# Performance work log

Measured on AMD Instinct MI355X. Metric: run time of the kernel, lower is better.

The kernel has to match this reference:

```python
import jax, jax.numpy as jnp
import numpy as np

N_MODELS = 128
N_FEAT = 32
TREE_LAYERS = [64, 32, 16]
INPUT_SIZE = 512
BATCH = 8192
EPS = 1e-5


def _uniform(key, shape, fan_in, fan_out):
    stdv = np.sqrt(6.0 / (fan_in + fan_out))
    return jax.random.uniform(key, shape, jnp.float32, -stdv, stdv)


def setup_inputs() -> dict:
    key = jax.random.key(0)
    ks = jax.random.split(key, 8)
    x = jax.random.normal(ks[0], (BATCH, INPUT_SIZE), jnp.float32)
    # flattened per-tree feature indices, shape [n_models * n_feature]
    used_features = jax.random.randint(ks[1], (N_MODELS * N_FEAT,), 0, INPUT_SIZE, jnp.int32)
    W1 = _uniform(ks[2], (N_MODELS, N_FEAT, TREE_LAYERS[0]), N_FEAT, TREE_LAYERS[0])
    b1 = jnp.zeros((N_MODELS, 1, TREE_LAYERS[0]), jnp.float32)
    W2 = _uniform(ks[3], (N_MODELS, TREE_LAYERS[0], TREE_LAYERS[1]), TREE_LAYERS[0], TREE_LAYERS[1])
    b2 = jnp.zeros((N_MODELS, 1, TREE_LAYERS[1]), jnp.float32)
    W3 = _uniform(ks[4], (N_MODELS, TREE_LAYERS[1], TREE_LAYERS[2]), TREE_LAYERS[1], TREE_LAYERS[2])
    b3 = jnp.zeros((N_MODELS, 1, TREE_LAYERS[2]), jnp.float32)
    gamma1 = jnp.ones((N_MODELS * TREE_LAYERS[0],), jnp.float32)
    beta1 = jnp.zeros((N_MODELS * TREE_LAYERS[0],), jnp.float32)
    gamma2 = jnp.ones((N_MODELS * TREE_LAYERS[1],), jnp.float32)
    beta2 = jnp.zeros((N_MODELS * TREE_LAYERS[1],), jnp.float32)
    out_weight = jax.random.normal(ks[5], (N_MODELS * TREE_LAYERS[2], 1), jnp.float32)
    out_bias = jnp.zeros((1,), jnp.float32)
    return {
        "x": x, "used_features": used_features,
        "W1": W1, "b1": b1, "W2": W2, "b2": b2, "W3": W3, "b3": b3,
        "gamma1": gamma1, "beta1": beta1, "gamma2": gamma2, "beta2": beta2,
        "out_weight": out_weight, "out_bias": out_bias,
    }


def _batch_dense(h, W, b):
    # h: [B, n_models, in], W: [n_models, in, out], b: [n_models, 1, out]
    return jnp.einsum("bmi,mio->bmo", h, W) + b[None, :, 0, :]


def _batchnorm_train(z, gamma, beta):
    # BatchNorm1d in training mode over 2D input: per-feature batch stats (biased var)
    mean = jnp.mean(z, axis=0)
    var = jnp.var(z, axis=0)
    return (z - mean) * jax.lax.rsqrt(var + EPS) * gamma + beta


def reference(x, used_features, W1, b1, W2, b2, W3, b3,
              gamma1, beta1, gamma2, beta2, out_weight, out_bias):
    B = x.shape[0]
    # gather used features: [B, n_models * n_feature] -> [B, n_models, n_feature]
    h = x[:, used_features].reshape(B, N_MODELS, N_FEAT)
    # layer 1: grouped GEMM + BN + ReLU
    h = _batch_dense(h, W1, b1).reshape(B, -1)
    h = jax.nn.relu(_batchnorm_train(h, gamma1, beta1))
    # layer 2
    h = _batch_dense(h.reshape(B, N_MODELS, -1), W2, b2).reshape(B, -1)
    h = jax.nn.relu(_batchnorm_train(h, gamma2, beta2))
    # last layer (no BN/ReLU) -> pred
    pred = _batch_dense(h.reshape(B, N_MODELS, -1), W3, b3).reshape(B, -1)
    out = pred @ out_weight + out_bias
    return (out, pred)
```

## Files before the change

kernel.cpp:

```cpp
#include <hip/hip_runtime.h>
#include <hip/hip_bf16.h>

#define BATCH   8192
#define NM      128
#define NF      32
#define L1      64
#define L2O     32
#define L3O     16
#define INSZ    512
#define SB      16
#define RPC     (BATCH/SB)
#define EPSV    1e-5f
#define CH      16
#define PARTS   (CH*4)

typedef __attribute__((ext_vector_type(8))) short short8;
typedef __attribute__((ext_vector_type(4))) float f32x4;

__device__ inline unsigned short f2bf(float f) {
    union { float f; unsigned u; } v; v.f = f;
    unsigned r = (v.u + 0x7FFF + ((v.u >> 16) & 1)) >> 16;
    return (unsigned short)r;
}


__global__ __launch_bounds__(256) void k_gather(
    const float* __restrict__ x, const int* __restrict__ uf,
    unsigned short* __restrict__ Ag)
{
    __shared__ float xs[16*INSZ];
    __shared__ int   sUf[NM*NF];
    const int rb = blockIdx.x;
    const int t  = threadIdx.x;
    const float4* xsrc = (const float4*)(x + (size_t)rb*16*INSZ);
    float4* xdst = (float4*)xs;
    #pragma unroll
    for (int p = 0; p < 8; ++p) xdst[t + p*256] = xsrc[t + p*256];
    const int4* us = (const int4*)uf;
    int4* ud = (int4*)sUf;
    #pragma unroll
    for (int p = 0; p < 4; ++p) ud[t + p*256] = us[t + p*256];
    __syncthreads();
    unsigned* outp = (unsigned*)(Ag + (size_t)rb*NM*512);
    const int e = t*2, r = e >> 5, j = e & 31;
    for (int m = 0; m < NM; ++m) {
        const int i0 = sUf[m*NF + j], i1 = sUf[m*NF + j + 1];
        const float g0 = xs[r*INSZ + i0], g1 = xs[r*INSZ + i1];
        outp[m*256 + t] = (unsigned)f2bf(g0) | ((unsigned)f2bf(g1) << 16);
    }
}

__global__ __launch_bounds__(256) void k_stats1_m(
    const unsigned short* __restrict__ Ag, const float* __restrict__ W1,
    float* __restrict__ sum1p, float* __restrict__ sq1p)
{
    const int m = blockIdx.x >> 4, chunk = blockIdx.x & 15;
    const int t = threadIdx.x, w = t >> 6, l = t & 63;
    const int lr = l & 15, lg = l >> 4;
    short8 w1f[4];
    #pragma unroll
    for (int n = 0; n < 4; ++n)
        #pragma unroll
        for (int s = 0; s < 8; ++s)
            w1f[n][s] = (short)f2bf(W1[(size_t)m*NF*L1 + (lg*8+s)*L1 + n*16 + lr]);
    float sum[4] = {0,0,0,0}, sq[4] = {0,0,0,0};
    for (int i = 0; i < 8; ++i) {
        const int rbG = chunk*32 + i*4 + w;
        const short8 a = *(const short8*)(Ag + ((size_t)rbG*NM + m)*512 + lr*32 + lg*8);
        #pragma unroll
        for (int n = 0; n < 4; ++n) {
            f32x4 acc = {0.f,0.f,0.f,0.f};
            acc = __builtin_amdgcn_mfma_f32_16x16x32_bf16(a, w1f[n], acc, 0, 0, 0);
            sum[n] += (acc[0]+acc[1]) + (acc[2]+acc[3]);
            sq[n]  += acc[0]*acc[0] + acc[1]*acc[1] + acc[2]*acc[2] + acc[3]*acc[3];
        }
    }
    #pragma unroll
    for (int n = 0; n < 4; ++n) {
        sum[n] += __shfl_xor(sum[n], 16); sum[n] += __shfl_xor(sum[n], 32);
        sq[n]  += __shfl_xor(sq[n], 16);  sq[n]  += __shfl_xor(sq[n], 32);
    }
    if (l < 16) {
        const int slot = chunk*4 + w;
        #pragma unroll
        for (int n = 0; n < 4; ++n) {
            const int f = m*L1 + n*16 + l;
            sum1p[(size_t)f*PARTS + slot] = sum[n];
            sq1p [(size_t)f*PARTS + slot] = sq[n];
        }
    }
}

__global__ __launch_bounds__(256) void k_finalize_m(
    const float* __restrict__ sump, const float* __restrict__ sqp,
    const float* __restrict__ bias, const float* __restrict__ gamma,
    const float* __restrict__ beta, float* __restrict__ scale,
    float* __restrict__ shift, int nfeat)
{
    int f = blockIdx.x*256 + threadIdx.x;
    if (f >= nfeat) return;
    float S = 0.f, Q = 0.f;
    #pragma unroll 8
    for (int c = 0; c < PARTS; ++c) { S += sump[(size_t)f*PARTS+c]; Q += sqp[(size_t)f*PARTS+c]; }
    float mz   = S * (1.f/BATCH);
    float var  = Q * (1.f/BATCH) - mz*mz;
    float mean = mz + bias[f];
    float sc   = rsqrtf(var + EPSV) * gamma[f];
    scale[f] = sc; shift[f] = beta[f] - mean*sc;
}

__global__ __launch_bounds__(256) void k_stats2_m(
    const unsigned short* __restrict__ Ag, const float* __restrict__ W1,
    const float* __restrict__ scale1, const float* __restrict__ shift1,
    const float* __restrict__ W2,
    float* __restrict__ sum2p, float* __restrict__ sq2p)
{
    __shared__ unsigned short h1T[4][16*72];
    const int m = blockIdx.x >> 4, chunk = blockIdx.x & 15;
    const int t = threadIdx.x, w = t >> 6, l = t & 63;
    const int lr = l & 15, lg = l >> 4;
    short8 w1f[4];
    #pragma unroll
    for (int n = 0; n < 4; ++n)
        #pragma unroll
        for (int s = 0; s < 8; ++s)
            w1f[n][s] = (short)f2bf(W1[(size_t)m*NF*L1 + (lg*8+s)*L1 + n*16 + lr]);
    float sc1[4], sh1[4];
    #pragma unroll
    for (int n = 0; n < 4; ++n) {
        sc1[n] = scale1[m*L1 + n*16 + lr];
        sh1[n] = shift1[m*L1 + n*16 + lr];
    }
    short8 w2f[2][2];
    #pragma unroll
    for (int n2 = 0; n2 < 2; ++n2)
        #pragma unroll
        for (int ks = 0; ks < 2; ++ks)
            #pragma unroll
            for (int s = 0; s < 8; ++s)
                w2f[n2][ks][s] = (short)f2bf(W2[(size_t)m*L1*L2O + (ks*32+lg*8+s)*L2O + n2*16 + lr]);
    unsigned short* hT = &h1T[w][0];
    float sum[2] = {0,0}, sq[2] = {0,0};
    for (int i = 0; i < 8; ++i) {
        const int rbG = chunk*32 + i*4 + w;
        const short8 a = *(const short8*)(Ag + ((size_t)rbG*NM + m)*512 + lr*32 + lg*8);
        #pragma unroll
        for (int n = 0; n < 4; ++n) {
            f32x4 acc = {0.f,0.f,0.f,0.f};
            acc = __builtin_amdgcn_mfma_f32_16x16x32_bf16(a, w1f[n], acc, 0, 0, 0);
            #pragma unroll
            for (int r = 0; r < 4; ++r) {
                float h = acc[r]*sc1[n] + sh1[n];
                hT[(lg*4+r)*72 + n*16 + lr] = f2bf(h > 0.f ? h : 0.f);
            }
        }
        #pragma unroll
        for (int n2 = 0; n2 < 2; ++n2) {
            f32x4 acc = {0.f,0.f,0.f,0.f};
            #pragma unroll
            for (int ks = 0; ks < 2; ++ks) {
                const short8 a2 = *(const short8*)(hT + lr*72 + ks*32 + lg*8);
                acc = __builtin_amdgcn_mfma_f32_16x16x32_bf16(a2, w2f[n2][ks], acc, 0, 0, 0);
            }
            sum[n2] += (acc[0]+acc[1]) + (acc[2]+acc[3]);
            sq[n2]  += acc[0]*acc[0] + acc[1]*acc[1] + acc[2]*acc[2] + acc[3]*acc[3];
        }
    }
    #pragma unroll
    for (int n2 = 0; n2 < 2; ++n2) {
        sum[n2] += __shfl_xor(sum[n2], 16); sum[n2] += __shfl_xor(sum[n2], 32);
        sq[n2]  += __shfl_xor(sq[n2], 16);  sq[n2]  += __shfl_xor(sq[n2], 32);
    }
    if (l < 16) {
        const int slot = chunk*4 + w;
        #pragma unroll
        for (int n2 = 0; n2 < 2; ++n2) {
            const int f = m*L2O + n2*16 + l;
            sum2p[(size_t)f*PARTS + slot] = sum[n2];
            sq2p [(size_t)f*PARTS + slot] = sq[n2];
        }
    }
}

__global__ __launch_bounds__(256) void k_final_m(
    const unsigned short* __restrict__ Ag, const float* __restrict__ W1,
    const float* __restrict__ scale1, const float* __restrict__ shift1,
    const float* __restrict__ W2,
    const float* __restrict__ scale2, const float* __restrict__ shift2,
    const float* __restrict__ W3, const float* __restrict__ b3,
    const float* __restrict__ ow,
    float* __restrict__ pred, float* __restrict__ outpart)
{
    __shared__ unsigned short h1T[4][16*72];
    __shared__ unsigned short h2T[4][16*40];
    const int m = blockIdx.x >> 4, chunk = blockIdx.x & 15;
    const int t = threadIdx.x, w = t >> 6, l = t & 63;
    const int lr = l & 15, lg = l >> 4;
    short8 w1f[4];
    #pragma unroll
    for (int n = 0; n < 4; ++n)
        #pragma unroll
        for (int s = 0; s < 8; ++s)
            w1f[n][s] = (short)f2bf(W1[(size_t)m*NF*L1 + (lg*8+s)*L1 + n*16 + lr]);
    float sc1[4], sh1[4];
    #pragma unroll
    for (int n = 0; n < 4; ++n) {
        sc1[n] = scale1[m*L1 + n*16 + lr];
        sh1[n] = shift1[m*L1 + n*16 + lr];
    }
    short8 w2f[2][2];
    #pragma unroll
    for (int n2 = 0; n2 < 2; ++n2)
        #pragma unroll
        for (int ks = 0; ks < 2; ++ks)
            #pragma unroll
            for (int s = 0; s < 8; ++s)
                w2f[n2][ks][s] = (short)f2bf(W2[(size_t)m*L1*L2O + (ks*32+lg*8+s)*L2O + n2*16 + lr]);
    float sc2[2], sh2[2];
    #pragma unroll
    for (int n2 = 0; n2 < 2; ++n2) {
        sc2[n2] = scale2[m*L2O + n2*16 + lr];
        sh2[n2] = shift2[m*L2O + n2*16 + lr];
    }
    short8 w3f;
    #pragma unroll
    for (int s = 0; s < 8; ++s)
        w3f[s] = (short)f2bf(W3[(size_t)m*L2O*L3O + (lg*8+s)*L3O + lr]);
    const float b3v = b3[m*L3O + lr];
    const float owv = ow[m*L3O + lr];
    unsigned short* hT  = &h1T[w][0];
    unsigned short* hT2 = &h2T[w][0];
    for (int i = 0; i < 8; ++i) {
        const int rbG = chunk*32 + i*4 + w;
        const short8 a = *(const short8*)(Ag + ((size_t)rbG*NM + m)*512 + lr*32 + lg*8);
        #pragma unroll
        for (int n = 0; n < 4; ++n) {
            f32x4 acc = {0.f,0.f,0.f,0.f};
            acc = __builtin_amdgcn_mfma_f32_16x16x32_bf16(a, w1f[n], acc, 0, 0, 0);
            #pragma unroll
            for (int r = 0; r < 4; ++r) {
                float h = acc[r]*sc1[n] + sh1[n];
                hT[(lg*4+r)*72 + n*16 + lr] = f2bf(h > 0.f ? h : 0.f);
            }
        }
        #pragma unroll
        for (int n2 = 0; n2 < 2; ++n2) {
            f32x4 acc = {0.f,0.f,0.f,0.f};
            #pragma unroll
            for (int ks = 0; ks < 2; ++ks) {
                const short8 a2 = *(const short8*)(hT + lr*72 + ks*32 + lg*8);
                acc = __builtin_amdgcn_mfma_f32_16x16x32_bf16(a2, w2f[n2][ks], acc, 0, 0, 0);
            }
            #pragma unroll
            for (int r = 0; r < 4; ++r) {
                float h = acc[r]*sc2[n2] + sh2[n2];
                hT2[(lg*4+r)*40 + n2*16 + lr] = f2bf(h > 0.f ? h : 0.f);
            }
        }
        {
            const short8 a3 = *(const short8*)(hT2 + lr*40 + lg*8);
            f32x4 acc = {0.f,0.f,0.f,0.f};
            acc = __builtin_amdgcn_mfma_f32_16x16x32_bf16(a3, w3f, acc, 0, 0, 0);
            #pragma unroll
            for (int r = 0; r < 4; ++r) {
                const float pv = acc[r] + b3v;
                const size_t row = (size_t)rbG*16 + lg*4 + r;
                pred[row*(NM*L3O) + m*L3O + lr] = pv;
                float v = pv * owv;
                v += __shfl_xor(v, 1); v += __shfl_xor(v, 2);
                v += __shfl_xor(v, 4); v += __shfl_xor(v, 8);
                if (lr == 0) outpart[row*NM + m] = v;
            }
        }
    }
}


__global__ __launch_bounds__(256) void k_stats1(
    const float* __restrict__ x, const int* __restrict__ uf,
    const float* __restrict__ W1, const float* __restrict__ b1,
    float* __restrict__ sum1p, float* __restrict__ sq1p)
{
    __shared__ __align__(16) float sW1[NF*L1];
    __shared__ __align__(16) float sFeat[8][NF];
    __shared__ int sIdx[NF];
    __shared__ float sRed[L1][4][2];
    const int m = blockIdx.x >> 4;
    const int c = blockIdx.x & (SB-1);
    const int t = threadIdx.x;
    for (int i = t; i < NF*L1; i += 256) sW1[i] = W1[m*NF*L1 + i];
    if (t < NF) sIdx[t] = uf[m*NF + t];
    __syncthreads();
    const int o = t & 63, r = t >> 6;
    float wcol[NF];
    #pragma unroll
    for (int i = 0; i < NF; ++i) wcol[i] = sW1[i*L1 + o];
    const float bias = b1[m*L1 + o];
    float sum = 0.f, sq = 0.f;
    const int row0 = c * RPC;
    const int rr = t >> 5, j = t & 31;
    for (int stage = 0; stage < RPC/8; ++stage) {
        __syncthreads();
        sFeat[rr][j] = x[(row0 + stage*8 + rr)*INSZ + sIdx[j]];
        __syncthreads();
        #pragma unroll
        for (int k = 0; k < 2; ++k) {
            const float4* fv = (const float4*)(&sFeat[r + k*4][0]);
            float acc = bias;
            #pragma unroll
            for (int ii = 0; ii < NF/4; ++ii) {
                float4 f4 = fv[ii];
                acc += f4.x*wcol[ii*4+0] + f4.y*wcol[ii*4+1]
                     + f4.z*wcol[ii*4+2] + f4.w*wcol[ii*4+3];
            }
            sum += acc; sq += acc*acc;
        }
    }
    sRed[o][r][0] = sum; sRed[o][r][1] = sq;
    __syncthreads();
    if (t < L1) {
        float S = 0.f, Q = 0.f;
        #pragma unroll
        for (int g = 0; g < 4; ++g) { S += sRed[t][g][0]; Q += sRed[t][g][1]; }
        sum1p[(m*L1 + t)*SB + c] = S;
        sq1p [(m*L1 + t)*SB + c] = Q;
    }
}

__global__ __launch_bounds__(256) void k_finalize(
    const float* __restrict__ sump, const float* __restrict__ sqp,
    const float* __restrict__ gamma, const float* __restrict__ beta,
    float* __restrict__ scale, float* __restrict__ shift, int nfeat)
{
    int f = blockIdx.x*256 + threadIdx.x;
    if (f >= nfeat) return;
    float S = 0.f, Q = 0.f;
    #pragma unroll
    for (int c = 0; c < SB; ++c) { S += sump[f*SB + c]; Q += sqp[f*SB + c]; }
    float mean = S * (1.f/BATCH);
    float var  = Q * (1.f/BATCH) - mean*mean;
    float rstd = rsqrtf(var + EPSV);
    float sc = rstd * gamma[f];
    scale[f] = sc;
    shift[f] = beta[f] - mean*sc;
}

__global__ __launch_bounds__(256) void k_stats2(
    const float* __restrict__ x, const int* __restrict__ uf,
    const float* __restrict__ W1, const float* __restrict__ b1,
    const float* __restrict__ scale1, const float* __restrict__ shift1,
    const float* __restrict__ W2, const float* __restrict__ b2,
    float* __restrict__ sum2p, float* __restrict__ sq2p)
{
    __shared__ __align__(16) float sW1[NF*L1];
    __shared__ __align__(16) float sFeat[8][NF];
    __shared__ __align__(16) float sH1[8][L1];
    __shared__ int sIdx[NF];
    __shared__ float sB1[L1], sSc[L1], sSh[L1];
    __shared__ float sRed[L2O][8][2];
    const int m = blockIdx.x >> 4, c = blockIdx.x & 15, t = threadIdx.x;
    for (int i = t; i < NF*L1; i += 256) sW1[i] = W1[m*NF*L1 + i];
    if (t < NF) sIdx[t] = uf[m*NF + t];
    if (t < L1) { sB1[t] = b1[m*L1+t]; sSc[t] = scale1[m*L1+t]; sSh[t] = shift1[m*L1+t]; }
    const int o2 = t & 31, r8 = t >> 5;
    float wcol2[L1];
    #pragma unroll
    for (int i = 0; i < L1; ++i) wcol2[i] = W2[m*L1*L2O + i*L2O + o2];
    const float b2v = b2[m*L2O + o2];
    __syncthreads();
    const int o1 = t & 63, r4 = t >> 6;
    float wcol1[NF];
    #pragma unroll
    for (int i = 0; i < NF; ++i) wcol1[i] = sW1[i*L1 + o1];
    const float b1v = sB1[o1], scv = sSc[o1], shv = sSh[o1];
    float sum = 0.f, sq = 0.f;
    const int row0 = c * RPC;
    const int rr = t >> 5, j = t & 31;
    for (int stage = 0; stage < RPC/8; ++stage) {
        __syncthreads();
        sFeat[rr][j] = x[(row0 + stage*8 + rr)*INSZ + sIdx[j]];
        __syncthreads();
        #pragma unroll
        for (int k = 0; k < 2; ++k) {
            const int rrow = r4 + k*4;
            const float4* fv = (const float4*)(&sFeat[rrow][0]);
            float acc = b1v;
            #pragma unroll
            for (int ii = 0; ii < NF/4; ++ii) {
                float4 f4 = fv[ii];
                acc += f4.x*wcol1[ii*4+0] + f4.y*wcol1[ii*4+1]
                     + f4.z*wcol1[ii*4+2] + f4.w*wcol1[ii*4+3];
            }
            float h = acc*scv + shv;
            sH1[rrow][o1] = h > 0.f ? h : 0.f;
        }
        __syncthreads();
        {
            const float4* hv = (const float4*)(&sH1[r8][0]);
            float acc = b2v;
            #pragma unroll
            for (int ii = 0; ii < L1/4; ++ii) {
                float4 h4 = hv[ii];
                acc += h4.x*wcol2[ii*4+0] + h4.y*wcol2[ii*4+1]
                     + h4.z*wcol2[ii*4+2] + h4.w*wcol2[ii*4+3];
            }
            sum += acc; sq += acc*acc;
        }
    }
    sRed[o2][r8][0] = sum; sRed[o2][r8][1] = sq;
    __syncthreads();
    if (t < L2O) {
        float S = 0.f, Q = 0.f;
        #pragma unroll
        for (int g = 0; g < 8; ++g) { S += sRed[t][g][0]; Q += sRed[t][g][1]; }
        sum2p[(m*L2O + t)*SB + c] = S;
        sq2p [(m*L2O + t)*SB + c] = Q;
    }
}

__global__ __launch_bounds__(256) void k_final(
    const float* __restrict__ x, const int* __restrict__ uf,
    const float* __restrict__ W1, const float* __restrict__ b1,
    const float* __restrict__ scale1, const float* __restrict__ shift1,
    const float* __restrict__ W2, const float* __restrict__ b2,
    const float* __restrict__ scale2, const float* __restrict__ shift2,
    const float* __restrict__ W3, const float* __restrict__ b3,
    const float* __restrict__ ow,
    float* __restrict__ pred, float* __restrict__ outpart)
{
    __shared__ __align__(16) float sW1[NF*L1];
    __shared__ __align__(16) float sFeat[8][NF];
    __shared__ __align__(16) float sH1[8][L1];
    __shared__ __align__(16) float sH2[8][L2O];
    __shared__ float sOut[8][L3O];
    __shared__ int sIdx[NF];
    __shared__ float sB1[L1], sSc[L1], sSh[L1];
    const int m = blockIdx.x >> 4, c = blockIdx.x & 15, t = threadIdx.x;
    for (int i = t; i < NF*L1; i += 256) sW1[i] = W1[m*NF*L1 + i];
    if (t < NF) sIdx[t] = uf[m*NF + t];
    if (t < L1) { sB1[t] = b1[m*L1+t]; sSc[t] = scale1[m*L1+t]; sSh[t] = shift1[m*L1+t]; }
    const int o2 = t & 31, r8 = t >> 5;
    float wcol2[L1];
    #pragma unroll
    for (int i = 0; i < L1; ++i) wcol2[i] = W2[m*L1*L2O + i*L2O + o2];
    const float b2v = b2[m*L2O + o2];
    const float sc2 = scale2[m*L2O + o2], sh2 = shift2[m*L2O + o2];
    const int o3 = t & 15, r16 = t >> 4;
    float wcol3[NF];
    #pragma unroll
    for (int i = 0; i < L2O; ++i) wcol3[i] = W3[m*L2O*L3O + i*L3O + o3];
    const float b3v = b3[m*L3O + o3];
    const float owv = ow[m*L3O + o3];
    __syncthreads();
    const int o1 = t & 63, r4 = t >> 6;
    float wcol1[NF];
    #pragma unroll
    for (int i = 0; i < NF; ++i) wcol1[i] = sW1[i*L1 + o1];
    const float b1v = sB1[o1], scv = sSc[o1], shv = sSh[o1];
    const int row0 = c * RPC;
    const int rr = t >> 5, j = t & 31;
    for (int stage = 0; stage < RPC/8; ++stage) {
        __syncthreads();
        sFeat[rr][j] = x[(row0 + stage*8 + rr)*INSZ + sIdx[j]];
        __syncthreads();
        #pragma unroll
        for (int k = 0; k < 2; ++k) {
            const int rrow = r4 + k*4;
            const float4* fv = (const float4*)(&sFeat[rrow][0]);
            float acc = b1v;
            #pragma unroll
            for (int ii = 0; ii < NF/4; ++ii) {
                float4 f4 = fv[ii];
                acc += f4.x*wcol1[ii*4+0] + f4.y*wcol1[ii*4+1]
                     + f4.z*wcol1[ii*4+2] + f4.w*wcol1[ii*4+3];
            }
            float h = acc*scv + shv;
            sH1[rrow][o1] = h > 0.f ? h : 0.f;
        }
        __syncthreads();
        {
            const float4* hv = (const float4*)(&sH1[r8][0]);
            float acc = b2v;
            #pragma unroll
            for (int ii = 0; ii < L1/4; ++ii) {
                float4 h4 = hv[ii];
                acc += h4.x*wcol2[ii*4+0] + h4.y*wcol2[ii*4+1]
                     + h4.z*wcol2[ii*4+2] + h4.w*wcol2[ii*4+3];
            }
            float h = acc*sc2 + sh2;
            sH2[r8][o2] = h > 0.f ? h : 0.f;
        }
        __syncthreads();
        if (t < 128) {
            const float4* hv = (const float4*)(&sH2[r16][0]);
            float acc = b3v;
            #pragma unroll
            for (int ii = 0; ii < L2O/4; ++ii) {
                float4 h4 = hv[ii];
                acc += h4.x*wcol3[ii*4+0] + h4.y*wcol3[ii*4+1]
                     + h4.z*wcol3[ii*4+2] + h4.w*wcol3[ii*4+3];
            }
            const int row = row0 + stage*8 + r16;
            pred[row*(NM*L3O) + m*L3O + o3] = acc;
            sOut[r16][o3] = acc * owv;
        }
        __syncthreads();
        if (t < 8) {
            float s = 0.f;
            #pragma unroll
            for (int i = 0; i < L3O; ++i) s += sOut[t][i];
            outpart[(row0 + stage*8 + t)*NM + m] = s;
        }
    }
}

__global__ __launch_bounds__(256) void k_out(
    const float* __restrict__ outpart, const float* __restrict__ ob,
    float* __restrict__ out)
{
    int b = blockIdx.x*256 + threadIdx.x;
    if (b >= BATCH) return;
    const float4* p = (const float4*)(outpart + (size_t)b*NM);
    float acc = 0.f;
    #pragma unroll
    for (int i = 0; i < NM/4; ++i) { float4 v = p[i]; acc += v.x + v.y + v.z + v.w; }
    out[b] = acc + ob[0];
}

extern "C" void kernel_launch(void* const* d_in, const int* in_sizes, int n_in,
                              void* d_out, int out_size, void* d_ws, size_t ws_size,
                              hipStream_t stream) {
    const float* x   = (const float*)d_in[0];
    const int*   uf  = (const int*  )d_in[1];
    const float* W1  = (const float*)d_in[2];
    const float* b1  = (const float*)d_in[3];
    const float* W2  = (const float*)d_in[4];
    const float* b2  = (const float*)d_in[5];
    const float* W3  = (const float*)d_in[6];
    const float* b3  = (const float*)d_in[7];
    const float* g1  = (const float*)d_in[8];
    const float* be1 = (const float*)d_in[9];
    const float* g2  = (const float*)d_in[10];
    const float* be2 = (const float*)d_in[11];
    const float* ow  = (const float*)d_in[12];
    const float* ob  = (const float*)d_in[13];

    float* out  = (float*)d_out;
    float* pred = out + BATCH;

    const size_t agElems = (size_t)BATCH * NM * NF;
    size_t need = agElems * 2;
    need += (size_t)(NM*L1*PARTS) * 4 * 2;
    need += (size_t)(NM*L2O*PARTS) * 4 * 2;
    need += (size_t)(NM*L1) * 4 * 2 + (size_t)(NM*L2O) * 4 * 2;
    need += (size_t)BATCH * NM * 4;

    if (ws_size >= need) {
        unsigned short* Ag = (unsigned short*)d_ws;
        float* w = (float*)(Ag + agElems);
        float* sum1p  = w;  w += NM*L1*PARTS;
        float* sq1p   = w;  w += NM*L1*PARTS;
        float* sum2p  = w;  w += NM*L2O*PARTS;
        float* sq2p   = w;  w += NM*L2O*PARTS;
        float* scale1 = w;  w += NM*L1;
        float* shift1 = w;  w += NM*L1;
        float* scale2 = w;  w += NM*L2O;
        float* shift2 = w;  w += NM*L2O;
        float* outpart= w;  w += (size_t)BATCH*NM;

        k_gather<<<BATCH/16, 256, 0, stream>>>(x, uf, Ag);
        k_stats1_m<<<NM*CH, 256, 0, stream>>>(Ag, W1, sum1p, sq1p);
        k_finalize_m<<<(NM*L1+255)/256, 256, 0, stream>>>(sum1p, sq1p, b1, g1, be1, scale1, shift1, NM*L1);
        k_stats2_m<<<NM*CH, 256, 0, stream>>>(Ag, W1, scale1, shift1, W2, sum2p, sq2p);
        k_finalize_m<<<(NM*L2O+255)/256, 256, 0, stream>>>(sum2p, sq2p, b2, g2, be2, scale2, shift2, NM*L2O);
        k_final_m<<<NM*CH, 256, 0, stream>>>(Ag, W1, scale1, shift1, W2, scale2, shift2,
                                             W3, b3, ow, pred, outpart);
        k_out<<<BATCH/256, 256, 0, stream>>>(outpart, ob, out);
    } else {
        float* w = (float*)d_ws;
        float* sum1p  = w;  w += NM*L1*SB;
        float* sq1p   = w;  w += NM*L1*SB;
        float* scale1 = w;  w += NM*L1;
        float* shift1 = w;  w += NM*L1;
        float* sum2p  = w;  w += NM*L2O*SB;
        float* sq2p   = w;  w += NM*L2O*SB;
        float* scale2 = w;  w += NM*L2O;
        float* shift2 = w;  w += NM*L2O;
        float* outpart= w;  w += (size_t)BATCH*NM;

        k_stats1<<<NM*SB, 256, 0, stream>>>(x, uf, W1, b1, sum1p, sq1p);
        k_finalize<<<(NM*L1+255)/256, 256, 0, stream>>>(sum1p, sq1p, g1, be1, scale1, shift1, NM*L1);
        k_stats2<<<NM*SB, 256, 0, stream>>>(x, uf, W1, b1, scale1, shift1, W2, b2, sum2p, sq2p);
        k_finalize<<<(NM*L2O+255)/256, 256, 0, stream>>>(sum2p, sq2p, g2, be2, scale2, shift2, NM*L2O);
        k_final<<<NM*SB, 256, 0, stream>>>(x, uf, W1, b1, scale1, shift1, W2, b2,
                                           scale2, shift2, W3, b3, ow, pred, outpart);
        k_out<<<BATCH/256, 256, 0, stream>>>(outpart, ob, out);
    }
}
```

Baseline: 116.3 us.

## Fuse gather with layer-1 stats and prepack bf16 MFMA weight fragments

Adds a prep kernel that converts W1/W2/W3 to bf16 in MFMA fragment order once per call, so the stats and final kernels load a short8 directly instead of doing per-element float loads and conversions. The gather kernel now also computes the layer-1 BatchNorm partial sums, converting x to bf16 in shared memory, which removes the separate stats1 pass over Ag. The output partial buffer is stored model-major so the final reduction reads coalesced, and the old ws-less fallback path is removed. The cost is more partial slots (256) for the stats1 finalize and one extra small launch.

```diff
diff --git a/kernel.cpp b/kernel.cpp
--- a/kernel.cpp
+++ b/kernel.cpp
@@ -8,21 +8,299 @@
 #define L2O     32
 #define L3O     16
 #define INSZ    512
-#define SB      16
-#define RPC     (BATCH/SB)
 #define EPSV    1e-5f
 #define CH      16
-#define PARTS   (CH*4)
+#define P64     64
+#define GS1B    256
+#define XS_STR  522
 
 typedef __attribute__((ext_vector_type(8))) short short8;
 typedef __attribute__((ext_vector_type(4))) float f32x4;
 
+union U8 { short8 s8; unsigned u[4]; };
+
 __device__ inline unsigned short f2bf(float f) {
     union { float f; unsigned u; } v; v.f = f;
-    unsigned r = (v.u + 0x7FFF + ((v.u >> 16) & 1)) >> 16;
-    return (unsigned short)r;
-}
-
+    return (unsigned short)((v.u + 0x7FFF + ((v.u >> 16) & 1)) >> 16);
+}
+__device__ inline unsigned pkbf(float a, float b) {
+    union { __hip_bfloat162 h; unsigned u; } c;
+    c.h = __float22bfloat162_rn(float2{a, b});
+    return c.u;
+}
+
+__global__ __launch_bounds__(256) void k_prep(
+    const float* __restrict__ W1, const float* __restrict__ W2,
+    const float* __restrict__ W3,
+    unsigned short* __restrict__ W1p, unsigned short* __restrict__ W2p,
+    unsigned short* __restrict__ W3p)
+{
+    int g = blockIdx.x*256 + threadIdx.x;
+    int m = g / 4608, r = g % 4608;
+    if (r < 2048) {
+        int n = r >> 9, l = (r >> 3) & 63, s = r & 7;
+        W1p[m*2048 + r] = f2bf(W1[m*2048 + ((l>>4)*8+s)*L1 + n*16 + (l&15)]);
+    } else if (r < 4096) {
+        int q = r - 2048;
+        int f = q >> 9, l = (q >> 3) & 63, s = q & 7;
+        int n2 = f >> 1, ks = f & 1;
+        W2p[m*2048 + q] = f2bf(W2[m*2048 + (ks*32+(l>>4)*8+s)*L2O + n2*16 + (l&15)]);
+    } else {
+        int q = r - 4096;
+        int l = (q >> 3) & 63, s = q & 7;
+        W3p[m*512 + q] = f2bf(W3[m*512 + ((l>>4)*8+s)*L3O + (l&15)]);
+    }
+}
+
+__global__ __launch_bounds__(512) void k_gs1(
+    const float* __restrict__ x, const int* __restrict__ uf,
+    const unsigned short* __restrict__ W1p,
+    unsigned short* __restrict__ Ag,
+    float* __restrict__ s1sum, float* __restrict__ s1sq)
+{
+    __shared__ unsigned short xs[32*XS_STR];
+    __shared__ int sUf[NM*NF];
+    const int blk = blockIdx.x, t = threadIdx.x;
+    #pragma unroll
+    for (int p = 0; p < 8; ++p) {
+        const float4 v = *(const float4*)(x + (size_t)blk*32*INSZ + p*2048 + t*4);
+        const int row = 4*p + (t>>7), col = (t&127)*4;
+        *(unsigned*)(&xs[row*XS_STR + col])     = pkbf(v.x, v.y);
+        *(unsigned*)(&xs[row*XS_STR + col + 2]) = pkbf(v.z, v.w);
+    }
+    #pragma unroll
+    for (int p = 0; p < 2; ++p)
+        ((int4*)sUf)[t + p*512] = ((const int4*)uf)[t + p*512];
+    __syncthreads();
+
+    const int w = t >> 6, l = t & 63, lr = l & 15, lg = l >> 4;
+    const unsigned short* xr0 = xs + lr*XS_STR;
+    const unsigned short* xr1 = xs + (16+lr)*XS_STR;
+    for (int mi = 0; mi < 16; ++mi) {
+        const int m = w*16 + mi;
+        const int4 ia = ((const int4*)sUf)[m*8 + lg*2];
+        const int4 ib = ((const int4*)sUf)[m*8 + lg*2 + 1];
+        U8 A0, A1;
+        A0.u[0] = xr0[ia.x] | ((unsigned)xr0[ia.y] << 16);
+        A0.u[1] = xr0[ia.z] | ((unsigned)xr0[ia.w] << 16);
+        A0.u[2] = xr0[ib.x] | ((unsigned)xr0[ib.y] << 16);
+        A0.u[3] = xr0[ib.z] | ((unsigned)xr0[ib.w] << 16);
+        A1.u[0] = xr1[ia.x] | ((unsigned)xr1[ia.y] << 16);
+        A1.u[1] = xr1[ia.z] | ((unsigned)xr1[ia.w] << 16);
+        A1.u[2] = xr1[ib.x] | ((unsigned)xr1[ib.y] << 16);
+        A1.u[3] = xr1[ib.z] | ((unsigned)xr1[ib.w] << 16);
+        *(short8*)(Ag + ((size_t)(blk*2  )*NM + m)*512 + lr*32 + lg*8) = A0.s8;
+        *(short8*)(Ag + ((size_t)(blk*2+1)*NM + m)*512 + lr*32 + lg*8) = A1.s8;
+        float sum[4], sq[4];
+        #pragma unroll
+        for (int n = 0; n < 4; ++n) {
+            const short8 wf = *(const short8*)(W1p + m*2048 + n*512 + l*8);
+            f32x4 z = {0.f,0.f,0.f,0.f};
+            f32x4 c0 = __builtin_amdgcn_mfma_f32_16x16x32_bf16(A0.s8, wf, z, 0, 0, 0);
+            f32x4 c1 = __builtin_amdgcn_mfma_f32_16x16x32_bf16(A1.s8, wf, z, 0, 0, 0);
+            sum[n] = (c0[0]+c0[1]) + (c0[2]+c0[3]) + (c1[0]+c1[1]) + (c1[2]+c1[3]);
+            sq[n]  = c0[0]*c0[0] + c0[1]*c0[1] + c0[2]*c0[2] + c0[3]*c0[3]
+                   + c1[0]*c1[0] + c1[1]*c1[1] + c1[2]*c1[2] + c1[3]*c1[3];
+        }
+        #pragma unroll
+        for (int n = 0; n < 4; ++n) {
+            sum[n] += __shfl_xor(sum[n], 16); sum[n] += __shfl_xor(sum[n], 32);
+            sq[n]  += __shfl_xor(sq[n], 16);  sq[n]  += __shfl_xor(sq[n], 32);
+        }
+        if (l < 16) {
+            #pragma unroll
+            for (int n = 0; n < 4; ++n) {
+                s1sum[(size_t)blk*8192 + m*64 + n*16 + l] = sum[n];
+                s1sq [(size_t)blk*8192 + m*64 + n*16 + l] = sq[n];
+            }
+        }
+    }
+}
+
+__global__ __launch_bounds__(256) void k_fin(
+    const float* __restrict__ sump, const float* __restrict__ sqp,
+    const float* __restrict__ bias, const float* __restrict__ gamma,
+    const float* __restrict__ beta, float* __restrict__ scale,
+    float* __restrict__ shift, int nfeat, int parts, int slotMajor)
+{
+    int f = blockIdx.x*256 + threadIdx.x;
+    if (f >= nfeat) return;
+    float S = 0.f, Q = 0.f;
+    if (slotMajor) {
+        #pragma unroll 8
+        for (int c = 0; c < parts; ++c) { S += sump[(size_t)c*nfeat + f]; Q += sqp[(size_t)c*nfeat + f]; }
+    } else {
+        #pragma unroll 8
+        for (int c = 0; c < parts; ++c) { S += sump[(size_t)f*parts + c]; Q += sqp[(size_t)f*parts + c]; }
+    }
+    float mz   = S * (1.f/BATCH);
+    float var  = Q * (1.f/BATCH) - mz*mz;
+    float mean = mz + bias[f];
+    float sc   = rsqrtf(var + EPSV) * gamma[f];
+    scale[f] = sc; shift[f] = beta[f] - mean*sc;
+}
+
+__global__ __launch_bounds__(256) void k_stats2_p(
+    const unsigned short* __restrict__ Ag, const unsigned short* __restrict__ W1p,
+    const float* __restrict__ scale1, const float* __restrict__ shift1,
+    const unsigned short* __restrict__ W2p,
+    float* __restrict__ sum2p, float* __restrict__ sq2p)
+{
+    __shared__ unsigned short h1T[4][16*72];
+    const int m = blockIdx.x >> 4, chunk = blockIdx.x & 15;
+    const int t = threadIdx.x, w = t >> 6, l = t & 63;
+    const int lr = l & 15, lg = l >> 4;
+    short8 w1f[4];
+    #pragma unroll
+    for (int n = 0; n < 4; ++n) w1f[n] = *(const short8*)(W1p + m*2048 + n*512 + l*8);
+    short8 w2f[2][2];
+    #pragma unroll
+    for (int n2 = 0; n2 < 2; ++n2)
+        #pragma unroll
+        for (int ks = 0; ks < 2; ++ks)
+            w2f[n2][ks] = *(const short8*)(W2p + m*2048 + (n2*2+ks)*512 + l*8);
+    float sc1[4], sh1[4];
+    #pragma unroll
+    for (int n = 0; n < 4; ++n) {
+        sc1[n] = scale1[m*L1 + n*16 + lr];
+        sh1[n] = shift1[m*L1 + n*16 + lr];
+    }
+    unsigned short* hT = &h1T[w][0];
+    float sum[2] = {0,0}, sq[2] = {0,0};
+    for (int i = 0; i < 8; ++i) {
+        const int rbG = chunk*32 + i*4 + w;
+        const short8 a = *(const short8*)(Ag + ((size_t)rbG*NM + m)*512 + lr*32 + lg*8);
+        #pragma unroll
+        for (int n = 0; n < 4; ++n) {
+            f32x4 acc = {0.f,0.f,0.f,0.f};
+            acc = __builtin_amdgcn_mfma_f32_16x16x32_bf16(a, w1f[n], acc, 0, 0, 0);
+            #pragma unroll
+            for (int r = 0; r < 4; ++r) {
+                float h = acc[r]*sc1[n] + sh1[n];
+                hT[(lg*4+r)*72 + n*16 + lr] = f2bf(h > 0.f ? h : 0.f);
+            }
+        }
+        #pragma unroll
+        for (int n2 = 0; n2 < 2; ++n2) {
+            f32x4 acc = {0.f,0.f,0.f,0.f};
+            #pragma unroll
+            for (int ks = 0; ks < 2; ++ks) {
+                const short8 a2 = *(const short8*)(hT + lr*72 + ks*32 + lg*8);
+                acc = __builtin_amdgcn_mfma_f32_16x16x32_bf16(a2, w2f[n2][ks], acc, 0, 0, 0);
+            }
+            sum[n2] += (acc[0]+acc[1]) + (acc[2]+acc[3]);
+            sq[n2]  += acc[0]*acc[0] + acc[1]*acc[1] + acc[2]*acc[2] + acc[3]*acc[3];
+        }
+    }
+    #pragma unroll
+    for (int n2 = 0; n2 < 2; ++n2) {
+        sum[n2] += __shfl_xor(sum[n2], 16); sum[n2] += __shfl_xor(sum[n2], 32);
+        sq[n2]  += __shfl_xor(sq[n2], 16);  sq[n2]  += __shfl_xor(sq[n2], 32);
+    }
+    if (l < 16) {
+        const int slot = chunk*4 + w;
+        #pragma unroll
+        for (int n2 = 0; n2 < 2; ++n2) {
+            const int f = m*L2O + n2*16 + l;
+            sum2p[(size_t)f*P64 + slot] = sum[n2];
+            sq2p [(size_t)f*P64 + slot] = sq[n2];
+        }
+    }
+}
+
+__global__ __launch_bounds__(256) void k_final_p(
+    const unsigned short* __restrict__ Ag, const unsigned short* __restrict__ W1p,
+    const float* __restrict__ scale1, const float* __restrict__ shift1,
+    const unsigned short* __restrict__ W2p,
+    const float* __restrict__ scale2, const float* __restrict__ shift2,
+    const unsigned short* __restrict__ W3p, const float* __restrict__ b3,
+    const float* __restrict__ ow,
+    float* __restrict__ pred, float* __restrict__ outpartT)
+{
+    __shared__ unsigned short h1T[4][16*72];
+    __shared__ unsigned short h2T[4][16*40];
+    const int m = blockIdx.x >> 4, chunk = blockIdx.x & 15;
+    const int t = threadIdx.x, w = t >> 6, l = t & 63;
+    const int lr = l & 15, lg = l >> 4;
+    short8 w1f[4];
+    #pragma unroll
+    for (int n = 0; n < 4; ++n) w1f[n] = *(const short8*)(W1p + m*2048 + n*512 + l*8);
+    short8 w2f[2][2];
+    #pragma unroll
+    for (int n2 = 0; n2 < 2; ++n2)
+        #pragma unroll
+        for (int ks = 0; ks < 2; ++ks)
+            w2f[n2][ks] = *(const short8*)(W2p + m*2048 + (n2*2+ks)*512 + l*8);
+    const short8 w3f = *(const short8*)(W3p + m*512 + l*8);
+    float sc1[4], sh1[4];
+    #pragma unroll
+    for (int n = 0; n < 4; ++n) {
+        sc1[n] = scale1[m*L1 + n*16 + lr];
+        sh1[n] = shift1[m*L1 + n*16 + lr];
+    }
+    float sc2[2], sh2[2];
+    #pragma unroll
+    for (int n2 = 0; n2 < 2; ++n2) {
+        sc2[n2] = scale2[m*L2O + n2*16 + lr];
+        sh2[n2] = shift2[m*L2O + n2*16 + lr];
+    }
+    const float4 b3f = *(const float4*)(b3 + m*L3O + lg*4);
+    const float4 owf = *(const float4*)(ow + m*L3O + lg*4);
+    unsigned short* hT  = &h1T[w][0];
+    unsigned short* hT2 = &h2T[w][0];
+    for (int i = 0; i < 8; ++i) {
+        const int rbG = chunk*32 + i*4 + w;
+        const short8 a = *(const short8*)(Ag + ((size_t)rbG*NM + m)*512 + lr*32 + lg*8);
+        #pragma unroll
+        for (int n = 0; n < 4; ++n) {
+            f32x4 acc = {0.f,0.f,0.f,0.f};
+            acc = __builtin_amdgcn_mfma_f32_16x16x32_bf16(a, w1f[n], acc, 0, 0, 0);
+            #pragma unroll
+            for (int r = 0; r < 4; ++r) {
+                float h = acc[r]*sc1[n] + sh1[n];
+                hT[(lg*4+r)*72 + n*16 + lr] = f2bf(h > 0.f ? h : 0.f);
+            }
+        }
+        #pragma unroll
+        for (int n2 = 0; n2 < 2; ++n2) {
+            f32x4 acc = {0.f,0.f,0.f,0.f};
+            #pragma unroll
+            for (int ks = 0; ks < 2; ++ks) {
+                const short8 a2 = *(const short8*)(hT + lr*72 + ks*32 + lg*8);
+                acc = __builtin_amdgcn_mfma_f32_16x16x32_bf16(a2, w2f[n2][ks], acc, 0, 0, 0);
+            }
+            #pragma unroll
+            for (int r = 0; r < 4; ++r) {
+                float h = acc[r]*sc2[n2] + sh2[n2];
+                hT2[(lg*4+r)*40 + n2*16 + lr] = f2bf(h > 0.f ? h : 0.f);
+            }
+        }
+        {
+            const short8 a3 = *(const short8*)(hT2 + lr*40 + lg*8);
+            f32x4 zz = {0.f,0.f,0.f,0.f};
+            f32x4 acc = __builtin_amdgcn_mfma_f32_16x16x32_bf16(w3f, a3, zz, 0, 0, 0);
+            float4 pv;
+            pv.x = acc[0] + b3f.x; pv.y = acc[1] + b3f.y;
+            pv.z = acc[2] + b3f.z; pv.w = acc[3] + b3f.w;
+            const size_t row = (size_t)rbG*16 + lr;
+            *(float4*)(pred + row*(NM*L3O) + m*L3O + lg*4) = pv;
+            float v = pv.x*owf.x + pv.y*owf.y + pv.z*owf.z + pv.w*owf.w;
+            v += __shfl_xor(v, 16); v += __shfl_xor(v, 32);
+            if (l < 16) outpartT[(size_t)m*BATCH + rbG*16 + l] = v;
+        }
+    }
+}
+
+__global__ __launch_bounds__(256) void k_outT(
+    const float* __restrict__ outpartT, const float* __restrict__ ob,
+    float* __restrict__ out)
+{
+    int b = blockIdx.x*256 + threadIdx.x;
+    float acc = ob[0];
+    #pragma unroll 8
+    for (int m = 0; m < NM; ++m) acc += outpartT[(size_t)m*BATCH + b];
+    out[b] = acc;
+}
 
 __global__ __launch_bounds__(256) void k_gather(
     const float* __restrict__ x, const int* __restrict__ uf,
@@ -45,13 +323,12 @@
     const int e = t*2, r = e >> 5, j = e & 31;
     for (int m = 0; m < NM; ++m) {
         const int i0 = sUf[m*NF + j], i1 = sUf[m*NF + j + 1];
-        const float g0 = xs[r*INSZ + i0], g1 = xs[r*INSZ + i1];
-        outp[m*256 + t] = (unsigned)f2bf(g0) | ((unsigned)f2bf(g1) << 16);
+        outp[m*256 + t] = pkbf(xs[r*INSZ + i0], xs[r*INSZ + i1]);
     }
 }
 
 __global__ __launch_bounds__(256) void k_stats1_m(
-    const unsigned short* __restrict__ Ag, const float* __restrict__ W1,
+    const unsigned short* __restrict__ Ag, const unsigned short* __restrict__ W1p,
     float* __restrict__ sum1p, float* __restrict__ sq1p)
 {
     const int m = blockIdx.x >> 4, chunk = blockIdx.x & 15;
@@ -59,10 +336,7 @@
     const int lr = l & 15, lg = l >> 4;
     short8 w1f[4];
     #pragma unroll
-    for (int n = 0; n < 4; ++n)
-        #pragma unroll
-        for (int s = 0; s < 8; ++s)
-            w1f[n][s] = (short)f2bf(W1[(size_t)m*NF*L1 + (lg*8+s)*L1 + n*16 + lr]);
+    for (int n = 0; n < 4; ++n) w1f[n] = *(const short8*)(W1p + m*2048 + n*512 + l*8);
     float sum[4] = {0,0,0,0}, sq[4] = {0,0,0,0};
     for (int i = 0; i < 8; ++i) {
         const int rbG = chunk*32 + i*4 + w;
@@ -85,446 +359,10 @@
         #pragma unroll
         for (int n = 0; n < 4; ++n) {
             const int f = m*L1 + n*16 + l;
-            sum1p[(size_t)f*PARTS + slot] = sum[n];
-            sq1p [(size_t)f*PARTS + slot] = sq[n];
-        }
-    }
-}
-
-__global__ __launch_bounds__(256) void k_finalize_m(
-    const float* __restrict__ sump, const float* __restrict__ sqp,
-    const float* __restrict__ bias, const float* __restrict__ gamma,
-    const float* __restrict__ beta, float* __restrict__ scale,
-    float* __restrict__ shift, int nfeat)
-{
-    int f = blockIdx.x*256 + threadIdx.x;
-    if (f >= nfeat) return;
-    float S = 0.f, Q = 0.f;
-    #pragma unroll 8
-    for (int c = 0; c < PARTS; ++c) { S += sump[(size_t)f*PARTS+c]; Q += sqp[(size_t)f*PARTS+c]; }
-    float mz   = S * (1.f/BATCH);
-    float var  = Q * (1.f/BATCH) - mz*mz;
-    float mean = mz + bias[f];
-    float sc   = rsqrtf(var + EPSV) * gamma[f];
-    scale[f] = sc; shift[f] = beta[f] - mean*sc;
-}
-
-__global__ __launch_bounds__(256) void k_stats2_m(
-    const unsigned short* __restrict__ Ag, const float* __restrict__ W1,
-    const float* __restrict__ scale1, const float* __restrict__ shift1,
-    const float* __restrict__ W2,
-    float* __restrict__ sum2p, float* __restrict__ sq2p)
-{
-    __shared__ unsigned short h1T[4][16*72];
-    const int m = blockIdx.x >> 4, chunk = blockIdx.x & 15;
-    const int t = threadIdx.x, w = t >> 6, l = t & 63;
-    const int lr = l & 15, lg = l >> 4;
-    short8 w1f[4];
-    #pragma unroll
-    for (int n = 0; n < 4; ++n)
-        #pragma unroll
-        for (int s = 0; s < 8; ++s)
-            w1f[n][s] = (short)f2bf(W1[(size_t)m*NF*L1 + (lg*8+s)*L1 + n*16 + lr]);
-    float sc1[4], sh1[4];
-    #pragma unroll
-    for (int n = 0; n < 4; ++n) {
-        sc1[n] = scale1[m*L1 + n*16 + lr];
-        sh1[n] = shift1[m*L1 + n*16 + lr];
-    }
-    short8 w2f[2][2];
-    #pragma unroll
-    for (int n2 = 0; n2 < 2; ++n2)
-        #pragma unroll
-        for (int ks = 0; ks < 2; ++ks)
-            #pragma unroll
-            for (int s = 0; s < 8; ++s)
-                w2f[n2][ks][s] = (short)f2bf(W2[(size_t)m*L1*L2O + (ks*32+lg*8+s)*L2O + n2*16 + lr]);
-    unsigned short* hT = &h1T[w][0];
-    float sum[2] = {0,0}, sq[2] = {0,0};
-    for (int i = 0; i < 8; ++i) {
-        const int rbG = chunk*32 + i*4 + w;
-        const short8 a = *(const short8*)(Ag + ((size_t)rbG*NM + m)*512 + lr*32 + lg*8);
-        #pragma unroll
-        for (int n = 0; n < 4; ++n) {
-            f32x4 acc = {0.f,0.f,0.f,0.f};
-            acc = __builtin_amdgcn_mfma_f32_16x16x32_bf16(a, w1f[n], acc, 0, 0, 0);
-            #pragma unroll
-            for (int r = 0; r < 4; ++r) {
-                float h = acc[r]*sc1[n] + sh1[n];
-                hT[(lg*4+r)*72 + n*16 + lr] = f2bf(h > 0.f ? h : 0.f);
-            }
-        }
-        #pragma unroll
-        for (int n2 = 0; n2 < 2; ++n2) {
-            f32x4 acc = {0.f,0.f,0.f,0.f};
-            #pragma unroll
-            for (int ks = 0; ks < 2; ++ks) {
-                const short8 a2 = *(const short8*)(hT + lr*72 + ks*32 + lg*8);
-                acc = __builtin_amdgcn_mfma_f32_16x16x32_bf16(a2, w2f[n2][ks], acc, 0, 0, 0);
-            }
-            sum[n2] += (acc[0]+acc[1]) + (acc[2]+acc[3]);
-            sq[n2]  += acc[0]*acc[0] + acc[1]*acc[1] + acc[2]*acc[2] + acc[3]*acc[3];
-        }
-    }
-    #pragma unroll
-    for (int n2 = 0; n2 < 2; ++n2) {
-        sum[n2] += __shfl_xor(sum[n2], 16); sum[n2] += __shfl_xor(sum[n2], 32);
-        sq[n2]  += __shfl_xor(sq[n2], 16);  sq[n2]  += __shfl_xor(sq[n2], 32);
-    }
-    if (l < 16) {
-        const int slot = chunk*4 + w;
-        #pragma unroll
-        for (int n2 = 0; n2 < 2; ++n2) {
-            const int f = m*L2O + n2*16 + l;
-            sum2p[(size_t)f*PARTS + slot] = sum[n2];
-            sq2p [(size_t)f*PARTS + slot] = sq[n2];
-        }
-    }
-}
-
-__global__ __launch_bounds__(256) void k_final_m(
-    const unsigned short* __restrict__ Ag, const float* __restrict__ W1,
-    const float* __restrict__ scale1, const float* __restrict__ shift1,
-    const float* __restrict__ W2,
-    const float* __restrict__ scale2, const float* __restrict__ shift2,
-    const float* __restrict__ W3, const float* __restrict__ b3,
-    const float* __restrict__ ow,
-    float* __restrict__ pred, float* __restrict__ outpart)
-{
-    __shared__ unsigned short h1T[4][16*72];
-    __shared__ unsigned short h2T[4][16*40];
-    const int m = blockIdx.x >> 4, chunk = blockIdx.x & 15;
-    const int t = threadIdx.x, w = t >> 6, l = t & 63;
-    const int lr = l & 15, lg = l >> 4;
-    short8 w1f[4];
-    #pragma unroll
-    for (int n = 0; n < 4; ++n)
-        #pragma unroll
-        for (int s = 0; s < 8; ++s)
-            w1f[n][s] = (short)f2bf(W1[(size_t)m*NF*L1 + (lg*8+s)*L1 + n*16 + lr]);
-    float sc1[4], sh1[4];
-    #pragma unroll
-    for (int n = 0; n < 4; ++n) {
-        sc1[n] = scale1[m*L1 + n*16 + lr];
-        sh1[n] = shift1[m*L1 + n*16 + lr];
-    }
-    short8 w2f[2][2];
-    #pragma unroll
-    for (int n2 = 0; n2 < 2; ++n2)
-        #pragma unroll
-        for (int ks = 0; ks < 2; ++ks)
-            #pragma unroll
-            for (int s = 0; s < 8; ++s)
-                w2f[n2][ks][s] = (short)f2bf(W2[(size_t)m*L1*L2O + (ks*32+lg*8+s)*L2O + n2*16 + lr]);
-    float sc2[2], sh2[2];
-    #pragma unroll
-    for (int n2 = 0; n2 < 2; ++n2) {
-        sc2[n2] = scale2[m*L2O + n2*16 + lr];
-        sh2[n2] = shift2[m*L2O + n2*16 + lr];
-    }
-    short8 w3f;
-    #pragma unroll
-    for (int s = 0; s < 8; ++s)
-        w3f[s] = (short)f2bf(W3[(size_t)m*L2O*L3O + (lg*8+s)*L3O + lr]);
-    const float b3v = b3[m*L3O + lr];
-    const float owv = ow[m*L3O + lr];
-    unsigned short* hT  = &h1T[w][0];
-    unsigned short* hT2 = &h2T[w][0];
-    for (int i = 0; i < 8; ++i) {
-        const int rbG = chunk*32 + i*4 + w;
-        const short8 a = *(const short8*)(Ag + ((size_t)rbG*NM + m)*512 + lr*32 + lg*8);
-        #pragma unroll
-        for (int n = 0; n < 4; ++n) {
-            f32x4 acc = {0.f,0.f,0.f,0.f};
-            acc = __builtin_amdgcn_mfma_f32_16x16x32_bf16(a, w1f[n], acc, 0, 0, 0);
-            #pragma unroll
-            for (int r = 0; r < 4; ++r) {
-                float h = acc[r]*sc1[n] + sh1[n];
-                hT[(lg*4+r)*72 + n*16 + lr] = f2bf(h > 0.f ? h : 0.f);
-            }
-        }
-        #pragma unroll
-        for (int n2 = 0; n2 < 2; ++n2) {
-            f32x4 acc = {0.f,0.f,0.f,0.f};
-            #pragma unroll
-            for (int ks = 0; ks < 2; ++ks) {
-                const short8 a2 = *(const short8*)(hT + lr*72 + ks*32 + lg*8);
-                acc = __builtin_amdgcn_mfma_f32_16x16x32_bf16(a2, w2f[n2][ks], acc, 0, 0, 0);
-            }
-            #pragma unroll
-            for (int r = 0; r < 4; ++r) {
-                float h = acc[r]*sc2[n2] + sh2[n2];
-                hT2[(lg*4+r)*40 + n2*16 + lr] = f2bf(h > 0.f ? h : 0.f);
-            }
-        }
-        {
-            const short8 a3 = *(const short8*)(hT2 + lr*40 + lg*8);
-            f32x4 acc = {0.f,0.f,0.f,0.f};
-            acc = __builtin_amdgcn_mfma_f32_16x16x32_bf16(a3, w3f, acc, 0, 0, 0);
-            #pragma unroll
-            for (int r = 0; r < 4; ++r) {
-                const float pv = acc[r] + b3v;
-                const size_t row = (size_t)rbG*16 + lg*4 + r;
-                pred[row*(NM*L3O) + m*L3O + lr] = pv;
-                float v = pv * owv;
-                v += __shfl_xor(v, 1); v += __shfl_xor(v, 2);
-                v += __shfl_xor(v, 4); v += __shfl_xor(v, 8);
-                if (lr == 0) outpart[row*NM + m] = v;
-            }
-        }
-    }
-}
-
-
-__global__ __launch_bounds__(256) void k_stats1(
-    const float* __restrict__ x, const int* __restrict__ uf,
-    const float* __restrict__ W1, const float* __restrict__ b1,
-    float* __restrict__ sum1p, float* __restrict__ sq1p)
-{
-    __shared__ __align__(16) float sW1[NF*L1];
-    __shared__ __align__(16) float sFeat[8][NF];
-    __shared__ int sIdx[NF];
-    __shared__ float sRed[L1][4][2];
-    const int m = blockIdx.x >> 4;
-    const int c = blockIdx.x & (SB-1);
-    const int t = threadIdx.x;
-    for (int i = t; i < NF*L1; i += 256) sW1[i] = W1[m*NF*L1 + i];
-    if (t < NF) sIdx[t] = uf[m*NF + t];
-    __syncthreads();
-    const int o = t & 63, r = t >> 6;
-    float wcol[NF];
-    #pragma unroll
-    for (int i = 0; i < NF; ++i) wcol[i] = sW1[i*L1 + o];
-    const float bias = b1[m*L1 + o];
-    float sum = 0.f, sq = 0.f;
-    const int row0 = c * RPC;
-    const int rr = t >> 5, j = t & 31;
-    for (int stage = 0; stage < RPC/8; ++stage) {
-        __syncthreads();
-        sFeat[rr][j] = x[(row0 + stage*8 + rr)*INSZ + sIdx[j]];
-        __syncthreads();
-        #pragma unroll
-        for (int k = 0; k < 2; ++k) {
-            const float4* fv = (const float4*)(&sFeat[r + k*4][0]);
-            float acc = bias;
-            #pragma unroll
-            for (int ii = 0; ii < NF/4; ++ii) {
-                float4 f4 = fv[ii];
-                acc += f4.x*wcol[ii*4+0] + f4.y*wcol[ii*4+1]
-                     + f4.z*wcol[ii*4+2] + f4.w*wcol[ii*4+3];
-            }
-            sum += acc; sq += acc*acc;
-        }
-    }
-    sRed[o][r][0] = sum; sRed[o][r][1] = sq;
-    __syncthreads();
-    if (t < L1) {
-        float S = 0.f, Q = 0.f;
-        #pragma unroll
-        for (int g = 0; g < 4; ++g) { S += sRed[t][g][0]; Q += sRed[t][g][1]; }
-        sum1p[(m*L1 + t)*SB + c] = S;
-        sq1p [(m*L1 + t)*SB + c] = Q;
-    }
-}
-
-__global__ __launch_bounds__(256) void k_finalize(
-    const float* __restrict__ sump, const float* __restrict__ sqp,
-    const float* __restrict__ gamma, const float* __restrict__ beta,
-    float* __restrict__ scale, float* __restrict__ shift, int nfeat)
-{
-    int f = blockIdx.x*256 + threadIdx.x;
-    if (f >= nfeat) return;
-    float S = 0.f, Q = 0.f;
-    #pragma unroll
-    for (int c = 0; c < SB; ++c) { S += sump[f*SB + c]; Q += sqp[f*SB + c]; }
-    float mean = S * (1.f/BATCH);
-    float var  = Q * (1.f/BATCH) - mean*mean;
-    float rstd = rsqrtf(var + EPSV);
-    float sc = rstd * gamma[f];
-    scale[f] = sc;
-    shift[f] = beta[f] - mean*sc;
-}
-
-__global__ __launch_bounds__(256) void k_stats2(
-    const float* __restrict__ x, const int* __restrict__ uf,
-    const float* __restrict__ W1, const float* __restrict__ b1,
-    const float* __restrict__ scale1, const float* __restrict__ shift1,
-    const float* __restrict__ W2, const float* __restrict__ b2,
-    float* __restrict__ sum2p, float* __restrict__ sq2p)
-{
-    __shared__ __align__(16) float sW1[NF*L1];
-    __shared__ __align__(16) float sFeat[8][NF];
-    __shared__ __align__(16) float sH1[8][L1];
-    __shared__ int sIdx[NF];
-    __shared__ float sB1[L1], sSc[L1], sSh[L1];
-    __shared__ float sRed[L2O][8][2];
-    const int m = blockIdx.x >> 4, c = blockIdx.x & 15, t = threadIdx.x;
-    for (int i = t; i < NF*L1; i += 256) sW1[i] = W1[m*NF*L1 + i];
-    if (t < NF) sIdx[t] = uf[m*NF + t];
-    if (t < L1) { sB1[t] = b1[m*L1+t]; sSc[t] = scale1[m*L1+t]; sSh[t] = shift1[m*L1+t]; }
-    const int o2 = t & 31, r8 = t >> 5;
-    float wcol2[L1];
-    #pragma unroll
-    for (int i = 0; i < L1; ++i) wcol2[i] = W2[m*L1*L2O + i*L2O + o2];
-    const float b2v = b2[m*L2O + o2];
-    __syncthreads();
-    const int o1 = t & 63, r4 = t >> 6;
-    float wcol1[NF];
-    #pragma unroll
-    for (int i = 0; i < NF; ++i) wcol1[i] = sW1[i*L1 + o1];
-    const float b1v = sB1[o1], scv = sSc[o1], shv = sSh[o1];
-    float sum = 0.f, sq = 0.f;
-    const int row0 = c * RPC;
-    const int rr = t >> 5, j = t & 31;
-    for (int stage = 0; stage < RPC/8; ++stage) {
-        __syncthreads();
-        sFeat[rr][j] = x[(row0 + stage*8 + rr)*INSZ + sIdx[j]];
-        __syncthreads();
-        #pragma unroll
-        for (int k = 0; k < 2; ++k) {
-            const int rrow = r4 + k*4;
-            const float4* fv = (const float4*)(&sFeat[rrow][0]);
-            float acc = b1v;
-            #pragma unroll
-            for (int ii = 0; ii < NF/4; ++ii) {
-                float4 f4 = fv[ii];
-                acc += f4.x*wcol1[ii*4+0] + f4.y*wcol1[ii*4+1]
-                     + f4.z*wcol1[ii*4+2] + f4.w*wcol1[ii*4+3];
-            }
-            float h = acc*scv + shv;
-            sH1[rrow][o1] = h > 0.f ? h : 0.f;
-        }
-        __syncthreads();
-        {
-            const float4* hv = (const float4*)(&sH1[r8][0]);
-            float acc = b2v;
-            #pragma unroll
-            for (int ii = 0; ii < L1/4; ++ii) {
-                float4 h4 = hv[ii];
-                acc += h4.x*wcol2[ii*4+0] + h4.y*wcol2[ii*4+1]
-                     + h4.z*wcol2[ii*4+2] + h4.w*wcol2[ii*4+3];
-            }
-            sum += acc; sq += acc*acc;
-        }
-    }
-    sRed[o2][r8][0] = sum; sRed[o2][r8][1] = sq;
-    __syncthreads();
-    if (t < L2O) {
-        float S = 0.f, Q = 0.f;
-        #pragma unroll
-        for (int g = 0; g < 8; ++g) { S += sRed[t][g][0]; Q += sRed[t][g][1]; }
-        sum2p[(m*L2O + t)*SB + c] = S;
-        sq2p [(m*L2O + t)*SB + c] = Q;
-    }
-}
-
-__global__ __launch_bounds__(256) void k_final(
-    const float* __restrict__ x, const int* __restrict__ uf,
-    const float* __restrict__ W1, const float* __restrict__ b1,
-    const float* __restrict__ scale1, const float* __restrict__ shift1,
-    const float* __restrict__ W2, const float* __restrict__ b2,
-    const float* __restrict__ scale2, const float* __restrict__ shift2,
-    const float* __restrict__ W3, const float* __restrict__ b3,
-    const float* __restrict__ ow,
-    float* __restrict__ pred, float* __restrict__ outpart)
-{
-    __shared__ __align__(16) float sW1[NF*L1];
-    __shared__ __align__(16) float sFeat[8][NF];
-    __shared__ __align__(16) float sH1[8][L1];
-    __shared__ __align__(16) float sH2[8][L2O];
-    __shared__ float sOut[8][L3O];
-    __shared__ int sIdx[NF];
-    __shared__ float sB1[L1], sSc[L1], sSh[L1];
-    const int m = blockIdx.x >> 4, c = blockIdx.x & 15, t = threadIdx.x;
-    for (int i = t; i < NF*L1; i += 256) sW1[i] = W1[m*NF*L1 + i];
-    if (t < NF) sIdx[t] = uf[m*NF + t];
-    if (t < L1) { sB1[t] = b1[m*L1+t]; sSc[t] = scale1[m*L1+t]; sSh[t] = shift1[m*L1+t]; }
-    const int o2 = t & 31, r8 = t >> 5;
-    float wcol2[L1];
-    #pragma unroll
-    for (int i = 0; i < L1; ++i) wcol2[i] = W2[m*L1*L2O + i*L2O + o2];
-    const float b2v = b2[m*L2O + o2];
-    const float sc2 = scale2[m*L2O + o2], sh2 = shift2[m*L2O + o2];
-    const int o3 = t & 15, r16 = t >> 4;
-    float wcol3[NF];
-    #pragma unroll
-    for (int i = 0; i < L2O; ++i) wcol3[i] = W3[m*L2O*L3O + i*L3O + o3];
-    const float b3v = b3[m*L3O + o3];
-    const float owv = ow[m*L3O + o3];
-    __syncthreads();
-    const int o1 = t & 63, r4 = t >> 6;
-    float wcol1[NF];
-    #pragma unroll
-    for (int i = 0; i < NF; ++i) wcol1[i] = sW1[i*L1 + o1];
-    const float b1v = sB1[o1], scv = sSc[o1], shv = sSh[o1];
-    const int row0 = c * RPC;
-    const int rr = t >> 5, j = t & 31;
-    for (int stage = 0; stage < RPC/8; ++stage) {
-        __syncthreads();
-        sFeat[rr][j] = x[(row0 + stage*8 + rr)*INSZ + sIdx[j]];
-        __syncthreads();
-        #pragma unroll
-        for (int k = 0; k < 2; ++k) {
-            const int rrow = r4 + k*4;
-            const float4* fv = (const float4*)(&sFeat[rrow][0]);
-            float acc = b1v;
-            #pragma unroll
-            for (int ii = 0; ii < NF/4; ++ii) {
-                float4 f4 = fv[ii];
-                acc += f4.x*wcol1[ii*4+0] + f4.y*wcol1[ii*4+1]
-                     + f4.z*wcol1[ii*4+2] + f4.w*wcol1[ii*4+3];
-            }
-            float h = acc*scv + shv;
-            sH1[rrow][o1] = h > 0.f ? h : 0.f;
-        }
-        __syncthreads();
-        {
-            const float4* hv = (const float4*)(&sH1[r8][0]);
-            float acc = b2v;
-            #pragma unroll
-            for (int ii = 0; ii < L1/4; ++ii) {
-                float4 h4 = hv[ii];
-                acc += h4.x*wcol2[ii*4+0] + h4.y*wcol2[ii*4+1]
-                     + h4.z*wcol2[ii*4+2] + h4.w*wcol2[ii*4+3];
-            }
-            float h = acc*sc2 + sh2;
-            sH2[r8][o2] = h > 0.f ? h : 0.f;
-        }
-        __syncthreads();
-        if (t < 128) {
-            const float4* hv = (const float4*)(&sH2[r16][0]);
-            float acc = b3v;
-            #pragma unroll
-            for (int ii = 0; ii < L2O/4; ++ii) {
-                float4 h4 = hv[ii];
-                acc += h4.x*wcol3[ii*4+0] + h4.y*wcol3[ii*4+1]
-                     + h4.z*wcol3[ii*4+2] + h4.w*wcol3[ii*4+3];
-            }
-            const int row = row0 + stage*8 + r16;
-            pred[row*(NM*L3O) + m*L3O + o3] = acc;
-            sOut[r16][o3] = acc * owv;
-        }
-        __syncthreads();
-        if (t < 8) {
-            float s = 0.f;
-            #pragma unroll
-            for (int i = 0; i < L3O; ++i) s += sOut[t][i];
-            outpart[(row0 + stage*8 + t)*NM + m] = s;
-        }
-    }
-}
-
-__global__ __launch_bounds__(256) void k_out(
-    const float* __restrict__ outpart, const float* __restrict__ ob,
-    float* __restrict__ out)
-{
-    int b = blockIdx.x*256 + threadIdx.x;
-    if (b >= BATCH) return;
-    const float4* p = (const float4*)(outpart + (size_t)b*NM);
-    float acc = 0.f;
-    #pragma unroll
-    for (int i = 0; i < NM/4; ++i) { float4 v = p[i]; acc += v.x + v.y + v.z + v.w; }
-    out[b] = acc + ob[0];
+            sum1p[(size_t)f*P64 + slot] = sum[n];
+            sq1p [(size_t)f*P64 + slot] = sq[n];
+        }
+    }
 }
 
 extern "C" void kernel_launch(void* const* d_in, const int* in_sizes, int n_in,
@@ -549,51 +387,53 @@
     float* pred = out + BATCH;
 
     const size_t agElems = (size_t)BATCH * NM * NF;
-    size_t need = agElems * 2;
-    need += (size_t)(NM*L1*PARTS) * 4 * 2;
-    need += (size_t)(NM*L2O*PARTS) * 4 * 2;
-    need += (size_t)(NM*L1) * 4 * 2 + (size_t)(NM*L2O) * 4 * 2;
-    need += (size_t)BATCH * NM * 4;
-
-    if (ws_size >= need) {
-        unsigned short* Ag = (unsigned short*)d_ws;
-        float* w = (float*)(Ag + agElems);
-        float* sum1p  = w;  w += NM*L1*PARTS;
-        float* sq1p   = w;  w += NM*L1*PARTS;
-        float* sum2p  = w;  w += NM*L2O*PARTS;
-        float* sq2p   = w;  w += NM*L2O*PARTS;
-        float* scale1 = w;  w += NM*L1;
-        float* shift1 = w;  w += NM*L1;
-        float* scale2 = w;  w += NM*L2O;
-        float* shift2 = w;  w += NM*L2O;
-        float* outpart= w;  w += (size_t)BATCH*NM;
+    unsigned short* Ag  = (unsigned short*)d_ws;
+    unsigned short* W1p = Ag + agElems;
+    unsigned short* W2p = W1p + NM*2048;
+    unsigned short* W3p = W2p + NM*2048;
+    float* scale1 = (float*)(W3p + NM*512);
+    float* shift1 = scale1 + NM*L1;
+    float* scale2 = shift1 + NM*L1;
+    float* shift2 = scale2 + NM*L2O;
+    float* arena  = shift2 + NM*L2O;
+    const size_t prefixBytes = (char*)arena - (char*)d_ws;
+
+    const size_t arenaA = (size_t)GS1B*8192*4*2;
+    const size_t s2Bytes = (size_t)NM*L2O*P64*4*2;
+    const size_t needA = prefixBytes + arenaA;
+    const size_t arenaB = (size_t)NM*L1*P64*4*2;
+    const size_t needB = prefixBytes + arenaB + s2Bytes;
+
+    k_prep<<<NM*4608/256, 256, 0, stream>>>(W1, W2, W3, W1p, W2p, W3p);
+
+    if (ws_size >= needA) {
+        float* s1sum = arena;
+        float* s1sq  = s1sum + (size_t)GS1B*8192;
+        float* s2sum = arena;
+        float* s2sq  = s2sum + (size_t)NM*L2O*P64;
+        float* outpartT = arena;
+
+        k_gs1<<<GS1B, 512, 0, stream>>>(x, uf, W1p, Ag, s1sum, s1sq);
+        k_fin<<<NM*L1/256, 256, 0, stream>>>(s1sum, s1sq, b1, g1, be1, scale1, shift1, NM*L1, GS1B, 1);
+        k_stats2_p<<<NM*CH, 256, 0, stream>>>(Ag, W1p, scale1, shift1, W2p, s2sum, s2sq);
+        k_fin<<<NM*L2O/256, 256, 0, stream>>>(s2sum, s2sq, b2, g2, be2, scale2, shift2, NM*L2O, P64, 0);
+        k_final_p<<<NM*CH, 256, 0, stream>>>(Ag, W1p, scale1, shift1, W2p, scale2, shift2,
+                                             W3p, b3, ow, pred, outpartT);
+        k_outT<<<BATCH/256, 256, 0, stream>>>(outpartT, ob, out);
+    } else {
+        float* s1sum = arena;
+        float* s1sq  = s1sum + (size_t)NM*L1*P64;
+        float* outpartT = arena;
+        float* s2sum = arena + arenaB/4;
+        float* s2sq  = s2sum + (size_t)NM*L2O*P64;
 
         k_gather<<<BATCH/16, 256, 0, stream>>>(x, uf, Ag);
-        k_stats1_m<<<NM*CH, 256, 0, stream>>>(Ag, W1, sum1p, sq1p);
-        k_finalize_m<<<(NM*L1+255)/256, 256, 0, stream>>>(sum1p, sq1p, b1, g1, be1, scale1, shift1, NM*L1);
-        k_stats2_m<<<NM*CH, 256, 0, stream>>>(Ag, W1, scale1, shift1, W2, sum2p, sq2p);
-        k_finalize_m<<<(NM*L2O+255)/256, 256, 0, stream>>>(sum2p, sq2p, b2, g2, be2, scale2, shift2, NM*L2O);
-        k_final_m<<<NM*CH, 256, 0, stream>>>(Ag, W1, scale1, shift1, W2, scale2, shift2,
-                                             W3, b3, ow, pred, outpart);
-        k_out<<<BATCH/256, 256, 0, stream>>>(outpart, ob, out);
-    } else {
-        float* w = (float*)d_ws;
-        float* sum1p  = w;  w += NM*L1*SB;
-        float* sq1p   = w;  w += NM*L1*SB;
-        float* scale1 = w;  w += NM*L1;
-        float* shift1 = w;  w += NM*L1;
-        float* sum2p  = w;  w += NM*L2O*SB;
-        float* sq2p   = w;  w += NM*L2O*SB;
-        float* scale2 = w;  w += NM*L2O;
-        float* shift2 = w;  w += NM*L2O;
-        float* outpart= w;  w += (size_t)BATCH*NM;
-
-        k_stats1<<<NM*SB, 256, 0, stream>>>(x, uf, W1, b1, sum1p, sq1p);
-        k_finalize<<<(NM*L1+255)/256, 256, 0, stream>>>(sum1p, sq1p, g1, be1, scale1, shift1, NM*L1);
-        k_stats2<<<NM*SB, 256, 0, stream>>>(x, uf, W1, b1, scale1, shift1, W2, b2, sum2p, sq2p);
-        k_finalize<<<(NM*L2O+255)/256, 256, 0, stream>>>(sum2p, sq2p, g2, be2, scale2, shift2, NM*L2O);
-        k_final<<<NM*SB, 256, 0, stream>>>(x, uf, W1, b1, scale1, shift1, W2, b2,
-                                           scale2, shift2, W3, b3, ow, pred, outpart);
-        k_out<<<BATCH/256, 256, 0, stream>>>(outpart, ob, out);
-    }
-}
+        k_stats1_m<<<NM*CH, 256, 0, stream>>>(Ag, W1p, s1sum, s1sq);
+        k_fin<<<NM*L1/256, 256, 0, stream>>>(s1sum, s1sq, b1, g1, be1, scale1, shift1, NM*L1, P64, 0);
+        k_stats2_p<<<NM*CH, 256, 0, stream>>>(Ag, W1p, scale1, shift1, W2p, s2sum, s2sq);
+        k_fin<<<NM*L2O/256, 256, 0, stream>>>(s2sum, s2sq, b2, g2, be2, scale2, shift2, NM*L2O, P64, 0);
+        k_final_p<<<NM*CH, 256, 0, stream>>>(Ag, W1p, scale1, shift1, W2p, scale2, shift2,
+                                             W3p, b3, ow, pred, outpartT);
+        k_outT<<<BATCH/256, 256, 0, stream>>>(outpartT, ob, out);
+    }
+}
```

Measured after the change: 107.5 us. 7.6% less time.
